# Kernel tuning notes

Measured on AMD Instinct MI355X. Metric: run time of the kernel, lower is better.

Reference implementation:

```python
import jax, jax.numpy as jnp
import numpy as np

# Dimensions (production-scale Qwen3-MoE-like, scaled for CPU exec)
T = 1024   # num_tokens
H = 1024   # hidden_size
F = 768    # moe_inter_padding_size (per-expert ffn dim)
E = 32     # expert_num (== num_local_experts, ep_size=1 -> expert_map is identity)
K = 4      # moe_k (top-k)


def setup_inputs() -> dict:
    key = jax.random.key(0)
    k1, k2, k3, k4 = jax.random.split(key, 4)
    hidden_states = jax.random.normal(k1, (T, H), jnp.float32)
    gate_w = jax.random.normal(k2, (E, H), jnp.float32) * 0.02       # router Linear weight (out,in)
    w1 = jax.random.normal(k3, (E, 2 * F, H), jnp.float32) * 0.02    # fused gate+up proj per expert
    w2 = jax.random.normal(k4, (E, H, F), jnp.float32) * 0.02        # down proj per expert
    return {"hidden_states": hidden_states, "gate_w": gate_w, "w1": w1, "w2": w2}


def reference(hidden_states, gate_w, w1, w2):
    # Router gate (logits computed in fp32, as in the torch code)
    router_logits = (hidden_states @ gate_w.T).astype(jnp.float32)      # [T, E]
    probs = jax.nn.softmax(router_logits, axis=-1)                      # [T, E]
    # SelectTopkOp: top-k over softmax probs, renormalize selected weights
    topk_w, topk_ids = jax.lax.top_k(probs, K)                          # [T, K]
    topk_w = topk_w / jnp.sum(topk_w, axis=-1, keepdims=True)
    # Dense combine weights: cw[t, e] = sum_k topk_w[t, k] * [topk_ids[t, k] == e]
    onehot = jax.nn.one_hot(topk_ids, E, dtype=topk_w.dtype)            # [T, K, E]
    cw = jnp.einsum("tk,tke->te", topk_w, onehot)                       # [T, E]
    # Grouped expert MLP with SiGLU: silu(gate) * up, then down proj
    gu = jnp.einsum("th,egh->etg", hidden_states, w1)                   # [E, T, 2F]
    g, u = gu[..., :F], gu[..., F:]
    act = jax.nn.silu(g) * u                                            # [E, T, F]
    y = jnp.einsum("etf,ehf->eth", act, w2)                             # [E, T, H]
    # Combine: weight each expert's output by its (sparse) routing weight
    out = jnp.einsum("eth,te->th", y, cw.astype(y.dtype))               # [T, H]
    return out
```

## Files before the change

kernel.cpp:

```cpp
#include <hip/hip_runtime.h>
#include <hip/hip_bf16.h>
#include <cmath>

#define TT 1024
#define HH 1024
#define FF 768
#define EE 32

typedef __bf16 bf16;
typedef __bf16 v8bf __attribute__((ext_vector_type(8)));
typedef float  v4f  __attribute__((ext_vector_type(4)));

static __device__ __forceinline__ v4f mfma16(v8bf a, v8bf b, v4f c) {
    return __builtin_amdgcn_mfma_f32_16x16x32_bf16(a, b, c, 0, 0, 0);
}

__global__ __launch_bounds__(64) void router_k(
    const float* __restrict__ x, const float* __restrict__ gw,
    bf16* __restrict__ xbf, int* __restrict__ tk_id, float* __restrict__ tk_w)
{
    int t = blockIdx.x, lane = threadIdx.x;
    float xr[16];
#pragma unroll
    for (int i = 0; i < 16; ++i) xr[i] = x[t * HH + i * 64 + lane];
#pragma unroll
    for (int i = 0; i < 16; ++i) xbf[t * HH + i * 64 + lane] = (bf16)xr[i];

    double acc[EE];
#pragma unroll
    for (int e = 0; e < EE; ++e) {
        double a = 0.0;
#pragma unroll
        for (int i = 0; i < 16; ++i)
            a += (double)xr[i] * (double)gw[e * HH + i * 64 + lane];
        acc[e] = a;
    }
#pragma unroll
    for (int m = 1; m < 64; m <<= 1) {
#pragma unroll
        for (int e = 0; e < EE; ++e) acc[e] += __shfl_xor(acc[e], m, 64);
    }
    if (lane == 0) {
        double mx = acc[0];
#pragma unroll
        for (int e = 1; e < EE; ++e) mx = fmax(mx, acc[e]);
        double p[EE];
        double s = 0.0;
#pragma unroll
        for (int e = 0; e < EE; ++e) { p[e] = exp(acc[e] - mx); s += p[e]; }
        int ids[4]; double w[4]; double ws = 0.0;
        for (int k = 0; k < 4; ++k) {
            int best = 0; double bv = -1.0;
            for (int e = 0; e < EE; ++e)
                if (p[e] > bv) { bv = p[e]; best = e; }
            ids[k] = best; w[k] = bv; ws += bv; p[best] = -2.0;
        }
        for (int k = 0; k < 4; ++k) {
            tk_id[t * 4 + k] = ids[k];
            tk_w[t * 4 + k] = (float)(w[k] / ws);
        }
    }
}

__global__ __launch_bounds__(1024) void scatter_k(
    const int* __restrict__ tk_id, const float* __restrict__ tk_w,
    int* __restrict__ cnt, int* __restrict__ offs,
    int* __restrict__ list, float* __restrict__ wlist)
{
    __shared__ int c_s[EE], o_s[EE], cur_s[EE];
    int tid = threadIdx.x;
    if (tid < EE) { c_s[tid] = 0; cur_s[tid] = 0; }
    __syncthreads();
    int ids[4]; float w[4];
#pragma unroll
    for (int k = 0; k < 4; ++k) { ids[k] = tk_id[tid * 4 + k]; w[k] = tk_w[tid * 4 + k]; }
#pragma unroll
    for (int k = 0; k < 4; ++k) atomicAdd(&c_s[ids[k]], 1);
    __syncthreads();
    if (tid == 0) {
        int a = 0;
        for (int e = 0; e < EE; ++e) { o_s[e] = a; a += c_s[e]; }
    }
    __syncthreads();
#pragma unroll
    for (int k = 0; k < 4; ++k) {
        int e = ids[k];
        int pos = atomicAdd(&cur_s[e], 1);
        int idx = o_s[e] + pos;
        list[idx] = tid * 4 + k;
        wlist[idx] = w[k];
    }
    if (tid < EE) { cnt[tid] = c_s[tid]; offs[tid] = o_s[tid]; }
    if (tid >= 1024 - 64) {
        list[4096 + (tid - 960)] = 0;
        wlist[4096 + (tid - 960)] = 0.f;
    }
}

__global__ __launch_bounds__(256) void gemm1_k(
    const bf16* __restrict__ xbf, const float* __restrict__ w1,
    const int* __restrict__ cnt, const int* __restrict__ offs,
    const int* __restrict__ list, bf16* __restrict__ act)
{
    int e = blockIdx.y, fb = blockIdx.x;
    int n = cnt[e];
    if (n == 0) return;
    int base = offs[e];

    __shared__ bf16 As[64][72];
    __shared__ bf16 Bs[128][72];

    int tid = threadIdx.x;
    int wid = tid >> 6, lane = tid & 63;
    int wr = wid >> 1, wc = wid & 1;
    int lrow = lane & 15, lk = (lane >> 4) * 8;
    const float* w1e = w1 + (size_t)e * 1536 * HH;

    int nm = (n + 63) >> 6;
    for (int mt = 0; mt < nm; ++mt) {
        v4f accg[2][2], accu[2][2];
#pragma unroll
        for (int m = 0; m < 2; ++m)
#pragma unroll
            for (int nf = 0; nf < 2; ++nf) { accg[m][nf] = (v4f)0.f; accu[m][nf] = (v4f)0.f; }

        for (int k0 = 0; k0 < HH; k0 += 64) {
#pragma unroll
            for (int it = 0; it < 2; ++it) {
                int idx = it * 256 + tid;
                int r = idx >> 3, oct = idx & 7;
                int code = list[base + mt * 64 + r];
                int tk = code >> 2;
                *(v8bf*)&As[r][oct * 8] =
                    *(const v8bf*)(xbf + (size_t)tk * HH + k0 + oct * 8);
            }
#pragma unroll
            for (int it = 0; it < 8; ++it) {
                int r = it * 16 + (tid >> 4);
                int q = tid & 15;
                int grow = (r < 64) ? (fb * 64 + r) : (768 + fb * 64 + (r - 64));
                float4 v = *(const float4*)(w1e + (size_t)grow * HH + k0 + q * 4);
                bf16* dst = &Bs[r][q * 4];
                dst[0] = (bf16)v.x; dst[1] = (bf16)v.y;
                dst[2] = (bf16)v.z; dst[3] = (bf16)v.w;
            }
            __syncthreads();
#pragma unroll
            for (int ks = 0; ks < 2; ++ks) {
                int kk = ks * 32 + lk;
                v8bf a0  = *(const v8bf*)&As[wr * 32 + lrow][kk];
                v8bf a1  = *(const v8bf*)&As[wr * 32 + 16 + lrow][kk];
                v8bf bg0 = *(const v8bf*)&Bs[wc * 32 + lrow][kk];
                v8bf bg1 = *(const v8bf*)&Bs[wc * 32 + 16 + lrow][kk];
                v8bf bu0 = *(const v8bf*)&Bs[64 + wc * 32 + lrow][kk];
                v8bf bu1 = *(const v8bf*)&Bs[64 + wc * 32 + 16 + lrow][kk];
                accg[0][0] = mfma16(a0, bg0, accg[0][0]);
                accg[0][1] = mfma16(a0, bg1, accg[0][1]);
                accg[1][0] = mfma16(a1, bg0, accg[1][0]);
                accg[1][1] = mfma16(a1, bg1, accg[1][1]);
                accu[0][0] = mfma16(a0, bu0, accu[0][0]);
                accu[0][1] = mfma16(a0, bu1, accu[0][1]);
                accu[1][0] = mfma16(a1, bu0, accu[1][0]);
                accu[1][1] = mfma16(a1, bu1, accu[1][1]);
            }
            __syncthreads();
        }
        int rb = wr * 32 + (lane >> 4) * 4;
#pragma unroll
        for (int m = 0; m < 2; ++m)
#pragma unroll
            for (int nf = 0; nf < 2; ++nf)
#pragma unroll
                for (int j = 0; j < 4; ++j) {
                    int r = mt * 64 + rb + m * 16 + j;
                    if (r < n) {
                        float g = accg[m][nf][j], u = accu[m][nf][j];
                        float a = g / (1.f + __expf(-g)) * u;
                        act[(size_t)(base + r) * FF + fb * 64 + wc * 32 + nf * 16 + lrow] = (bf16)a;
                    }
                }
    }
}

__global__ __launch_bounds__(256) void gemm2_k(
    const bf16* __restrict__ act, const float* __restrict__ w2,
    const int* __restrict__ cnt, const int* __restrict__ offs,
    const int* __restrict__ list, const float* __restrict__ wlist,
    float* __restrict__ ybuf)
{
    int e = blockIdx.y, hb = blockIdx.x;
    int n = cnt[e];
    if (n == 0) return;
    int base = offs[e];

    __shared__ bf16 As[64][72];
    __shared__ bf16 Bs[64][72];

    int tid = threadIdx.x;
    int wid = tid >> 6, lane = tid & 63;
    int wr = wid >> 1, wc = wid & 1;
    int lrow = lane & 15, lk = (lane >> 4) * 8;
    const float* w2e = w2 + (size_t)e * HH * FF;

    int nm = (n + 63) >> 6;
    for (int mt = 0; mt < nm; ++mt) {
        v4f acc[2][2];
#pragma unroll
        for (int m = 0; m < 2; ++m)
#pragma unroll
            for (int nf = 0; nf < 2; ++nf) acc[m][nf] = (v4f)0.f;

        for (int k0 = 0; k0 < FF; k0 += 64) {
#pragma unroll
            for (int it = 0; it < 2; ++it) {
                int idx = it * 256 + tid;
                int r = idx >> 3, oct = idx & 7;
                *(v8bf*)&As[r][oct * 8] =
                    *(const v8bf*)(act + (size_t)(base + mt * 64 + r) * FF + k0 + oct * 8);
            }
#pragma unroll
            for (int it = 0; it < 4; ++it) {
                int r = it * 16 + (tid >> 4);
                int q = tid & 15;
                float4 v = *(const float4*)(w2e + (size_t)(hb * 64 + r) * FF + k0 + q * 4);
                bf16* dst = &Bs[r][q * 4];
                dst[0] = (bf16)v.x; dst[1] = (bf16)v.y;
                dst[2] = (bf16)v.z; dst[3] = (bf16)v.w;
            }
            __syncthreads();
#pragma unroll
            for (int ks = 0; ks < 2; ++ks) {
                int kk = ks * 32 + lk;
                v8bf a0 = *(const v8bf*)&As[wr * 32 + lrow][kk];
                v8bf a1 = *(const v8bf*)&As[wr * 32 + 16 + lrow][kk];
                v8bf b0 = *(const v8bf*)&Bs[wc * 32 + lrow][kk];
                v8bf b1 = *(const v8bf*)&Bs[wc * 32 + 16 + lrow][kk];
                acc[0][0] = mfma16(a0, b0, acc[0][0]);
                acc[0][1] = mfma16(a0, b1, acc[0][1]);
                acc[1][0] = mfma16(a1, b0, acc[1][0]);
                acc[1][1] = mfma16(a1, b1, acc[1][1]);
            }
            __syncthreads();
        }
        int rb = wr * 32 + (lane >> 4) * 4;
#pragma unroll
        for (int m = 0; m < 2; ++m)
#pragma unroll
            for (int j = 0; j < 4; ++j) {
                int r = mt * 64 + rb + m * 16 + j;
                if (r < n) {
                    int code = list[base + r];
                    float w = wlist[base + r];
#pragma unroll
                    for (int nf = 0; nf < 2; ++nf) {
                        int col = wc * 32 + nf * 16 + lrow;
                        ybuf[(size_t)code * HH + hb * 64 + col] = acc[m][nf][j] * w;
                    }
                }
            }
    }
}

__global__ __launch_bounds__(256) void combine_k(
    const float* __restrict__ ybuf, float* __restrict__ out)
{
    int idx = blockIdx.x * 256 + threadIdx.x;
    int t = idx >> 8, c = idx & 255;
    const float4* yb = (const float4*)ybuf;
    float4 a = yb[(size_t)(t * 4 + 0) * 256 + c];
    float4 b = yb[(size_t)(t * 4 + 1) * 256 + c];
    float4 d = yb[(size_t)(t * 4 + 2) * 256 + c];
    float4 e = yb[(size_t)(t * 4 + 3) * 256 + c];
    float4 s;
    s.x = a.x + b.x + d.x + e.x;
    s.y = a.y + b.y + d.y + e.y;
    s.z = a.z + b.z + d.z + e.z;
    s.w = a.w + b.w + d.w + e.w;
    ((float4*)out)[(size_t)t * 256 + c] = s;
}

extern "C" void kernel_launch(void* const* d_in, const int* in_sizes, int n_in,
                              void* d_out, int out_size, void* d_ws, size_t ws_size,
                              hipStream_t stream)
{
    const float* x  = (const float*)d_in[0];
    const float* gw = (const float*)d_in[1];
    const float* w1 = (const float*)d_in[2];
    const float* w2 = (const float*)d_in[3];
    float* out = (float*)d_out;

    char* ws = (char*)d_ws;
    size_t off = 0;
    auto alloc = [&](size_t bytes) {
        void* p = ws + off;
        off = (off + bytes + 255) & ~(size_t)255;
        return p;
    };
    bf16*  xbf   = (bf16*) alloc((size_t)TT * HH * 2);
    int*   tk_id = (int*)  alloc(4096 * 4);
    float* tk_w  = (float*)alloc(4096 * 4);
    int*   cnt   = (int*)  alloc(EE * 4);
    int*   offs  = (int*)  alloc(EE * 4);
    int*   list  = (int*)  alloc(4160 * 4);
    float* wlist = (float*)alloc(4160 * 4);
    bf16*  act   = (bf16*) alloc((size_t)4160 * FF * 2);
    float* ybuf  = (float*)alloc((size_t)4096 * HH * 4);

    router_k<<<TT, 64, 0, stream>>>(x, gw, xbf, tk_id, tk_w);
    scatter_k<<<1, 1024, 0, stream>>>(tk_id, tk_w, cnt, offs, list, wlist);
    gemm1_k<<<dim3(12, EE), 256, 0, stream>>>(xbf, w1, cnt, offs, list, act);
    gemm2_k<<<dim3(16, EE), 256, 0, stream>>>(act, w2, cnt, offs, list, wlist, ybuf);
    combine_k<<<1024, 256, 0, stream>>>(ybuf, out);
}
```

Before: 470.3 us.

## Flatten expert M-tiles into a global tile list and vectorize router loads

The scatter kernel now builds a compact list of (expert, m-tile) pairs, and both grouped GEMMs launch one block per (tile, column block) with an XCD-aware block-index swizzle instead of looping over m-tiles inside each per-expert block. This spreads uneven expert loads across many more blocks and removes the serial m-tile loop. The router is changed to use float4 loads and to take top-k over logits before a softmax on only the four selected values, skipping the full 32-way exp. Tiles beyond MAXTILE=96 are silently dropped, which is safe only while the total tile count stays within that bound.

Result: slower. 482.2 us (+2.5%).

```diff
diff --git a/kernel.cpp b/kernel.cpp
--- a/kernel.cpp
+++ b/kernel.cpp
@@ -6,8 +6,10 @@
 #define HH 1024
 #define FF 768
 #define EE 32
+#define MAXTILE 96
 
 typedef __bf16 bf16;
+typedef __bf16 v4bf __attribute__((ext_vector_type(4)));
 typedef __bf16 v8bf __attribute__((ext_vector_type(8)));
 typedef float  v4f  __attribute__((ext_vector_type(4)));
 
@@ -20,19 +22,27 @@
     bf16* __restrict__ xbf, int* __restrict__ tk_id, float* __restrict__ tk_w)
 {
     int t = blockIdx.x, lane = threadIdx.x;
-    float xr[16];
-#pragma unroll
-    for (int i = 0; i < 16; ++i) xr[i] = x[t * HH + i * 64 + lane];
-#pragma unroll
-    for (int i = 0; i < 16; ++i) xbf[t * HH + i * 64 + lane] = (bf16)xr[i];
+    float4 xr[4];
+    const float4* xrow = (const float4*)(x + (size_t)t * HH);
+#pragma unroll
+    for (int i = 0; i < 4; ++i) xr[i] = xrow[i * 64 + lane];
+#pragma unroll
+    for (int i = 0; i < 4; ++i) {
+        v4bf b = { (bf16)xr[i].x, (bf16)xr[i].y, (bf16)xr[i].z, (bf16)xr[i].w };
+        *(v4bf*)(xbf + (size_t)t * HH + (i * 64 + lane) * 4) = b;
+    }
 
     double acc[EE];
 #pragma unroll
     for (int e = 0; e < EE; ++e) {
+        const float4* grow = (const float4*)(gw + (size_t)e * HH);
         double a = 0.0;
 #pragma unroll
-        for (int i = 0; i < 16; ++i)
-            a += (double)xr[i] * (double)gw[e * HH + i * 64 + lane];
+        for (int i = 0; i < 4; ++i) {
+            float4 g = grow[i * 64 + lane];
+            a += (double)xr[i].x * g.x + (double)xr[i].y * g.y
+               + (double)xr[i].z * g.z + (double)xr[i].w * g.w;
+        }
         acc[e] = a;
     }
 #pragma unroll
@@ -41,23 +51,18 @@
         for (int e = 0; e < EE; ++e) acc[e] += __shfl_xor(acc[e], m, 64);
     }
     if (lane == 0) {
-        double mx = acc[0];
-#pragma unroll
-        for (int e = 1; e < EE; ++e) mx = fmax(mx, acc[e]);
-        double p[EE];
-        double s = 0.0;
-#pragma unroll
-        for (int e = 0; e < EE; ++e) { p[e] = exp(acc[e] - mx); s += p[e]; }
-        int ids[4]; double w[4]; double ws = 0.0;
+        int ids[4]; double lv[4];
         for (int k = 0; k < 4; ++k) {
-            int best = 0; double bv = -1.0;
+            int best = 0; double bv = -1.0e300;
             for (int e = 0; e < EE; ++e)
-                if (p[e] > bv) { bv = p[e]; best = e; }
-            ids[k] = best; w[k] = bv; ws += bv; p[best] = -2.0;
-        }
+                if (acc[e] > bv) { bv = acc[e]; best = e; }
+            ids[k] = best; lv[k] = bv; acc[best] = -2.0e300;
+        }
+        double w[4], s = 0.0;
+        for (int k = 0; k < 4; ++k) { w[k] = exp(lv[k] - lv[0]); s += w[k]; }
         for (int k = 0; k < 4; ++k) {
             tk_id[t * 4 + k] = ids[k];
-            tk_w[t * 4 + k] = (float)(w[k] / ws);
+            tk_w[t * 4 + k] = (float)(w[k] / s);
         }
     }
 }
@@ -65,7 +70,8 @@
 __global__ __launch_bounds__(1024) void scatter_k(
     const int* __restrict__ tk_id, const float* __restrict__ tk_w,
     int* __restrict__ cnt, int* __restrict__ offs,
-    int* __restrict__ list, float* __restrict__ wlist)
+    int* __restrict__ list, float* __restrict__ wlist,
+    int* __restrict__ tile_e, int* __restrict__ tile_m)
 {
     __shared__ int c_s[EE], o_s[EE], cur_s[EE];
     int tid = threadIdx.x;
@@ -80,6 +86,10 @@
     if (tid == 0) {
         int a = 0;
         for (int e = 0; e < EE; ++e) { o_s[e] = a; a += c_s[e]; }
+        int nt = 0;
+        for (int e = 0; e < EE; ++e)
+            for (int m = 0; m * 64 < c_s[e]; ++m) { tile_e[nt] = e; tile_m[nt] = m; ++nt; }
+        for (int i = nt; i < MAXTILE; ++i) { tile_e[i] = -1; tile_m[i] = 0; }
     }
     __syncthreads();
 #pragma unroll
@@ -100,11 +110,16 @@
 __global__ __launch_bounds__(256) void gemm1_k(
     const bf16* __restrict__ xbf, const float* __restrict__ w1,
     const int* __restrict__ cnt, const int* __restrict__ offs,
-    const int* __restrict__ list, bf16* __restrict__ act)
-{
-    int e = blockIdx.y, fb = blockIdx.x;
+    const int* __restrict__ list, const int* __restrict__ tile_e,
+    const int* __restrict__ tile_m, bf16* __restrict__ act)
+{
+    int id = blockIdx.x;
+    int p = (id & 7) * 144 + (id >> 3);
+    int fb = p / MAXTILE, tl = p % MAXTILE;
+    int e = tile_e[tl];
+    if (e < 0) return;
+    int mt = tile_m[tl];
     int n = cnt[e];
-    if (n == 0) return;
     int base = offs[e];
 
     __shared__ bf16 As[64][72];
@@ -116,81 +131,80 @@
     int lrow = lane & 15, lk = (lane >> 4) * 8;
     const float* w1e = w1 + (size_t)e * 1536 * HH;
 
-    int nm = (n + 63) >> 6;
-    for (int mt = 0; mt < nm; ++mt) {
-        v4f accg[2][2], accu[2][2];
-#pragma unroll
-        for (int m = 0; m < 2; ++m)
-#pragma unroll
-            for (int nf = 0; nf < 2; ++nf) { accg[m][nf] = (v4f)0.f; accu[m][nf] = (v4f)0.f; }
-
-        for (int k0 = 0; k0 < HH; k0 += 64) {
-#pragma unroll
-            for (int it = 0; it < 2; ++it) {
-                int idx = it * 256 + tid;
-                int r = idx >> 3, oct = idx & 7;
-                int code = list[base + mt * 64 + r];
-                int tk = code >> 2;
-                *(v8bf*)&As[r][oct * 8] =
-                    *(const v8bf*)(xbf + (size_t)tk * HH + k0 + oct * 8);
+    int r0 = tid >> 3, r1 = 32 + (tid >> 3), oct = tid & 7;
+    int tk0 = list[base + mt * 64 + r0] >> 2;
+    int tk1 = list[base + mt * 64 + r1] >> 2;
+
+    v4f accg[2][2], accu[2][2];
+#pragma unroll
+    for (int m = 0; m < 2; ++m)
+#pragma unroll
+        for (int nf = 0; nf < 2; ++nf) { accg[m][nf] = (v4f)0.f; accu[m][nf] = (v4f)0.f; }
+
+    for (int k0 = 0; k0 < HH; k0 += 64) {
+        *(v8bf*)&As[r0][oct * 8] = *(const v8bf*)(xbf + (size_t)tk0 * HH + k0 + oct * 8);
+        *(v8bf*)&As[r1][oct * 8] = *(const v8bf*)(xbf + (size_t)tk1 * HH + k0 + oct * 8);
+#pragma unroll
+        for (int it = 0; it < 8; ++it) {
+            int r = it * 16 + (tid >> 4);
+            int q = tid & 15;
+            int grow = (r < 64) ? (fb * 64 + r) : (768 + fb * 64 + (r - 64));
+            float4 v = *(const float4*)(w1e + (size_t)grow * HH + k0 + q * 4);
+            bf16* dst = &Bs[r][q * 4];
+            dst[0] = (bf16)v.x; dst[1] = (bf16)v.y;
+            dst[2] = (bf16)v.z; dst[3] = (bf16)v.w;
+        }
+        __syncthreads();
+#pragma unroll
+        for (int ks = 0; ks < 2; ++ks) {
+            int kk = ks * 32 + lk;
+            v8bf a0  = *(const v8bf*)&As[wr * 32 + lrow][kk];
+            v8bf a1  = *(const v8bf*)&As[wr * 32 + 16 + lrow][kk];
+            v8bf bg0 = *(const v8bf*)&Bs[wc * 32 + lrow][kk];
+            v8bf bg1 = *(const v8bf*)&Bs[wc * 32 + 16 + lrow][kk];
+            v8bf bu0 = *(const v8bf*)&Bs[64 + wc * 32 + lrow][kk];
+            v8bf bu1 = *(const v8bf*)&Bs[64 + wc * 32 + 16 + lrow][kk];
+            accg[0][0] = mfma16(a0, bg0, accg[0][0]);
+            accg[0][1] = mfma16(a0, bg1, accg[0][1]);
+            accg[1][0] = mfma16(a1, bg0, accg[1][0]);
+            accg[1][1] = mfma16(a1, bg1, accg[1][1]);
+            accu[0][0] = mfma16(a0, bu0, accu[0][0]);
+            accu[0][1] = mfma16(a0, bu1, accu[0][1]);
+            accu[1][0] = mfma16(a1, bu0, accu[1][0]);
+            accu[1][1] = mfma16(a1, bu1, accu[1][1]);
+        }
+        __syncthreads();
+    }
+    int rb = wr * 32 + (lane >> 4) * 4;
+#pragma unroll
+    for (int m = 0; m < 2; ++m)
+#pragma unroll
+        for (int nf = 0; nf < 2; ++nf)
+#pragma unroll
+            for (int j = 0; j < 4; ++j) {
+                int r = mt * 64 + rb + m * 16 + j;
+                if (r < n) {
+                    float g = accg[m][nf][j], u = accu[m][nf][j];
+                    float a = g / (1.f + __expf(-g)) * u;
+                    act[(size_t)(base + r) * FF + fb * 64 + wc * 32 + nf * 16 + lrow] = (bf16)a;
+                }
             }
-#pragma unroll
-            for (int it = 0; it < 8; ++it) {
-                int r = it * 16 + (tid >> 4);
-                int q = tid & 15;
-                int grow = (r < 64) ? (fb * 64 + r) : (768 + fb * 64 + (r - 64));
-                float4 v = *(const float4*)(w1e + (size_t)grow * HH + k0 + q * 4);
-                bf16* dst = &Bs[r][q * 4];
-                dst[0] = (bf16)v.x; dst[1] = (bf16)v.y;
-                dst[2] = (bf16)v.z; dst[3] = (bf16)v.w;
-            }
-            __syncthreads();
-#pragma unroll
-            for (int ks = 0; ks < 2; ++ks) {
-                int kk = ks * 32 + lk;
-                v8bf a0  = *(const v8bf*)&As[wr * 32 + lrow][kk];
-                v8bf a1  = *(const v8bf*)&As[wr * 32 + 16 + lrow][kk];
-                v8bf bg0 = *(const v8bf*)&Bs[wc * 32 + lrow][kk];
-                v8bf bg1 = *(const v8bf*)&Bs[wc * 32 + 16 + lrow][kk];
-                v8bf bu0 = *(const v8bf*)&Bs[64 + wc * 32 + lrow][kk];
-                v8bf bu1 = *(const v8bf*)&Bs[64 + wc * 32 + 16 + lrow][kk];
-                accg[0][0] = mfma16(a0, bg0, accg[0][0]);
-                accg[0][1] = mfma16(a0, bg1, accg[0][1]);
-                accg[1][0] = mfma16(a1, bg0, accg[1][0]);
-                accg[1][1] = mfma16(a1, bg1, accg[1][1]);
-                accu[0][0] = mfma16(a0, bu0, accu[0][0]);
-                accu[0][1] = mfma16(a0, bu1, accu[0][1]);
-                accu[1][0] = mfma16(a1, bu0, accu[1][0]);
-                accu[1][1] = mfma16(a1, bu1, accu[1][1]);
-            }
-            __syncthreads();
-        }
-        int rb = wr * 32 + (lane >> 4) * 4;
-#pragma unroll
-        for (int m = 0; m < 2; ++m)
-#pragma unroll
-            for (int nf = 0; nf < 2; ++nf)
-#pragma unroll
-                for (int j = 0; j < 4; ++j) {
-                    int r = mt * 64 + rb + m * 16 + j;
-                    if (r < n) {
-                        float g = accg[m][nf][j], u = accu[m][nf][j];
-                        float a = g / (1.f + __expf(-g)) * u;
-                        act[(size_t)(base + r) * FF + fb * 64 + wc * 32 + nf * 16 + lrow] = (bf16)a;
-                    }
-                }
-    }
 }
 
 __global__ __launch_bounds__(256) void gemm2_k(
     const bf16* __restrict__ act, const float* __restrict__ w2,
     const int* __restrict__ cnt, const int* __restrict__ offs,
     const int* __restrict__ list, const float* __restrict__ wlist,
+    const int* __restrict__ tile_e, const int* __restrict__ tile_m,
     float* __restrict__ ybuf)
 {
-    int e = blockIdx.y, hb = blockIdx.x;
+    int id = blockIdx.x;
+    int p = (id & 7) * 192 + (id >> 3);
+    int hb = p / MAXTILE, tl = p % MAXTILE;
+    int e = tile_e[tl];
+    if (e < 0) return;
+    int mt = tile_m[tl];
     int n = cnt[e];
-    if (n == 0) return;
     int base = offs[e];
 
     __shared__ bf16 As[64][72];
@@ -202,63 +216,59 @@
     int lrow = lane & 15, lk = (lane >> 4) * 8;
     const float* w2e = w2 + (size_t)e * HH * FF;
 
-    int nm = (n + 63) >> 6;
-    for (int mt = 0; mt < nm; ++mt) {
-        v4f acc[2][2];
-#pragma unroll
-        for (int m = 0; m < 2; ++m)
-#pragma unroll
-            for (int nf = 0; nf < 2; ++nf) acc[m][nf] = (v4f)0.f;
-
-        for (int k0 = 0; k0 < FF; k0 += 64) {
-#pragma unroll
-            for (int it = 0; it < 2; ++it) {
-                int idx = it * 256 + tid;
-                int r = idx >> 3, oct = idx & 7;
-                *(v8bf*)&As[r][oct * 8] =
-                    *(const v8bf*)(act + (size_t)(base + mt * 64 + r) * FF + k0 + oct * 8);
-            }
-#pragma unroll
-            for (int it = 0; it < 4; ++it) {
-                int r = it * 16 + (tid >> 4);
-                int q = tid & 15;
-                float4 v = *(const float4*)(w2e + (size_t)(hb * 64 + r) * FF + k0 + q * 4);
-                bf16* dst = &Bs[r][q * 4];
-                dst[0] = (bf16)v.x; dst[1] = (bf16)v.y;
-                dst[2] = (bf16)v.z; dst[3] = (bf16)v.w;
-            }
-            __syncthreads();
-#pragma unroll
-            for (int ks = 0; ks < 2; ++ks) {
-                int kk = ks * 32 + lk;
-                v8bf a0 = *(const v8bf*)&As[wr * 32 + lrow][kk];
-                v8bf a1 = *(const v8bf*)&As[wr * 32 + 16 + lrow][kk];
-                v8bf b0 = *(const v8bf*)&Bs[wc * 32 + lrow][kk];
-                v8bf b1 = *(const v8bf*)&Bs[wc * 32 + 16 + lrow][kk];
-                acc[0][0] = mfma16(a0, b0, acc[0][0]);
-                acc[0][1] = mfma16(a0, b1, acc[0][1]);
-                acc[1][0] = mfma16(a1, b0, acc[1][0]);
-                acc[1][1] = mfma16(a1, b1, acc[1][1]);
-            }
-            __syncthreads();
-        }
-        int rb = wr * 32 + (lane >> 4) * 4;
-#pragma unroll
-        for (int m = 0; m < 2; ++m)
-#pragma unroll
-            for (int j = 0; j < 4; ++j) {
-                int r = mt * 64 + rb + m * 16 + j;
-                if (r < n) {
-                    int code = list[base + r];
-                    float w = wlist[base + r];
-#pragma unroll
-                    for (int nf = 0; nf < 2; ++nf) {
-                        int col = wc * 32 + nf * 16 + lrow;
-                        ybuf[(size_t)code * HH + hb * 64 + col] = acc[m][nf][j] * w;
-                    }
+    int r0 = tid >> 3, r1 = 32 + (tid >> 3), oct = tid & 7;
+    const bf16* arow0 = act + (size_t)(base + mt * 64 + r0) * FF;
+    const bf16* arow1 = act + (size_t)(base + mt * 64 + r1) * FF;
+
+    v4f acc[2][2];
+#pragma unroll
+    for (int m = 0; m < 2; ++m)
+#pragma unroll
+        for (int nf = 0; nf < 2; ++nf) acc[m][nf] = (v4f)0.f;
+
+    for (int k0 = 0; k0 < FF; k0 += 64) {
+        *(v8bf*)&As[r0][oct * 8] = *(const v8bf*)(arow0 + k0 + oct * 8);
+        *(v8bf*)&As[r1][oct * 8] = *(const v8bf*)(arow1 + k0 + oct * 8);
+#pragma unroll
+        for (int it = 0; it < 4; ++it) {
+            int r = it * 16 + (tid >> 4);
+            int q = tid & 15;
+            float4 v = *(const float4*)(w2e + (size_t)(hb * 64 + r) * FF + k0 + q * 4);
+            bf16* dst = &Bs[r][q * 4];
+            dst[0] = (bf16)v.x; dst[1] = (bf16)v.y;
+            dst[2] = (bf16)v.z; dst[3] = (bf16)v.w;
+        }
+        __syncthreads();
+#pragma unroll
+        for (int ks = 0; ks < 2; ++ks) {
+            int kk = ks * 32 + lk;
+            v8bf a0 = *(const v8bf*)&As[wr * 32 + lrow][kk];
+            v8bf a1 = *(const v8bf*)&As[wr * 32 + 16 + lrow][kk];
+            v8bf b0 = *(const v8bf*)&Bs[wc * 32 + lrow][kk];
+            v8bf b1 = *(const v8bf*)&Bs[wc * 32 + 16 + lrow][kk];
+            acc[0][0] = mfma16(a0, b0, acc[0][0]);
+            acc[0][1] = mfma16(a0, b1, acc[0][1]);
+            acc[1][0] = mfma16(a1, b0, acc[1][0]);
+            acc[1][1] = mfma16(a1, b1, acc[1][1]);
+        }
+        __syncthreads();
+    }
+    int rb = wr * 32 + (lane >> 4) * 4;
+#pragma unroll
+    for (int m = 0; m < 2; ++m)
+#pragma unroll
+        for (int j = 0; j < 4; ++j) {
+            int r = mt * 64 + rb + m * 16 + j;
+            if (r < n) {
+                int code = list[base + r];
+                float w = wlist[base + r];
+#pragma unroll
+                for (int nf = 0; nf < 2; ++nf) {
+                    int col = wc * 32 + nf * 16 + lrow;
+                    ybuf[(size_t)code * HH + hb * 64 + col] = acc[m][nf][j] * w;
                 }
             }
-    }
+        }
 }
 
 __global__ __launch_bounds__(256) void combine_k(
@@ -296,19 +306,21 @@
         off = (off + bytes + 255) & ~(size_t)255;
         return p;
     };
-    bf16*  xbf   = (bf16*) alloc((size_t)TT * HH * 2);
-    int*   tk_id = (int*)  alloc(4096 * 4);
-    float* tk_w  = (float*)alloc(4096 * 4);
-    int*   cnt   = (int*)  alloc(EE * 4);
-    int*   offs  = (int*)  alloc(EE * 4);
-    int*   list  = (int*)  alloc(4160 * 4);
-    float* wlist = (float*)alloc(4160 * 4);
-    bf16*  act   = (bf16*) alloc((size_t)4160 * FF * 2);
-    float* ybuf  = (float*)alloc((size_t)4096 * HH * 4);
+    bf16*  xbf    = (bf16*) alloc((size_t)TT * HH * 2);
+    int*   tk_id  = (int*)  alloc(4096 * 4);
+    float* tk_w   = (float*)alloc(4096 * 4);
+    int*   cnt    = (int*)  alloc(EE * 4);
+    int*   offs   = (int*)  alloc(EE * 4);
+    int*   list   = (int*)  alloc(4160 * 4);
+    float* wlist  = (float*)alloc(4160 * 4);
+    int*   tile_e = (int*)  alloc(MAXTILE * 4);
+    int*   tile_m = (int*)  alloc(MAXTILE * 4);
+    bf16*  act    = (bf16*) alloc((size_t)4160 * FF * 2);
+    float* ybuf   = (float*)alloc((size_t)4096 * HH * 4);
 
     router_k<<<TT, 64, 0, stream>>>(x, gw, xbf, tk_id, tk_w);
-    scatter_k<<<1, 1024, 0, stream>>>(tk_id, tk_w, cnt, offs, list, wlist);
-    gemm1_k<<<dim3(12, EE), 256, 0, stream>>>(xbf, w1, cnt, offs, list, act);
-    gemm2_k<<<dim3(16, EE), 256, 0, stream>>>(act, w2, cnt, offs, list, wlist, ybuf);
+    scatter_k<<<1, 1024, 0, stream>>>(tk_id, tk_w, cnt, offs, list, wlist, tile_e, tile_m);
+    gemm1_k<<<MAXTILE * 12, 256, 0, stream>>>(xbf, w1, cnt, offs, list, tile_e, tile_m, act);
+    gemm2_k<<<MAXTILE * 16, 256, 0, stream>>>(act, w2, cnt, offs, list, wlist, tile_e, tile_m, ybuf);
     combine_k<<<1024, 256, 0, stream>>>(ybuf, out);
 }
```
